# Optimization experiments

Measured on AMD Instinct MI355X. Metric: run time of the kernel, lower is better.

## Reference

```python
import jax, jax.numpy as jnp
import numpy as np

B, S, D, H = 1, 2048, 1024, 16
DH = D // H  # 64
ROPE_THETA = 10000.0


def _rope_tables(seq_len, half_dim, theta):
    inv = 1.0 / (theta ** (np.arange(0, half_dim, dtype=np.float32) / half_dim))
    ang = np.arange(seq_len, dtype=np.float32)[:, None] * inv[None, :]
    return jnp.asarray(np.cos(ang)), jnp.asarray(np.sin(ang))


def setup_inputs() -> dict:
    key = jax.random.key(0)
    ks = jax.random.split(key, 6)
    x = jax.random.normal(ks[0], (B, S, D), dtype=jnp.float32)
    # block-diagonal mask over ~4 packed images -> sorted segment ids
    seg_ids = jnp.sort(jax.random.randint(ks[1], (S,), 0, 4, dtype=jnp.int32))
    freqs_cos, freqs_sin = _rope_tables(S, DH // 2, ROPE_THETA)
    scale = 1.0 / np.sqrt(D)
    wq = jax.random.normal(ks[2], (D, D), dtype=jnp.float32) * scale
    wk = jax.random.normal(ks[3], (D, D), dtype=jnp.float32) * scale
    wv = jax.random.normal(ks[4], (D, D), dtype=jnp.float32) * scale
    wo = jax.random.normal(ks[5], (D, D), dtype=jnp.float32) * scale
    return {"x": x, "seg_ids": seg_ids, "freqs_cos": freqs_cos,
            "freqs_sin": freqs_sin, "wq": wq, "wk": wk, "wv": wv, "wo": wo}


def _apply_rope(t, cos, sin):
    # t: [B,S,H,DH]; interpret last dim as DH//2 complex pairs (real, imag)
    tr = t.reshape(B, S, H, DH // 2, 2)
    a, b = tr[..., 0], tr[..., 1]
    c = cos[None, :, None, :]  # [1,S,1,DH/2]
    s = sin[None, :, None, :]
    out = jnp.stack([a * c - b * s, a * s + b * c], axis=-1)
    return out.reshape(B, S, H, DH)


def reference(x, seg_ids, freqs_cos, freqs_sin, wq, wk, wv, wo):
    q = (x @ wq.T).reshape(B, S, H, DH)
    k = (x @ wk.T).reshape(B, S, H, DH)
    v = (x @ wv.T).reshape(B, S, H, DH)
    q = _apply_rope(q, freqs_cos, freqs_sin)
    k = _apply_rope(k, freqs_cos, freqs_sin)
    scores = jnp.einsum('bqhd,bkhd->bhqk', q, k) / np.float32(np.sqrt(DH))
    block_mask = (seg_ids[:, None] == seg_ids[None, :])  # [S,S] block-diagonal
    scores = jnp.where(block_mask[None, None], scores, jnp.float32(-1e9))
    attn = jax.nn.softmax(scores, axis=-1)
    out = jnp.einsum('bhqk,bkhd->bqhd', attn, v).reshape(B, S, D)
    return out @ wo.T
```

## Files before the change

### kernel.cpp

```cpp
#include <hip/hip_runtime.h>

typedef __bf16 bf16;
typedef __bf16 bf16x4 __attribute__((ext_vector_type(4)));
typedef __bf16 bf16x8 __attribute__((ext_vector_type(8)));
typedef float  f32x4  __attribute__((ext_vector_type(4)));
typedef _Float16 f16;
typedef f16 f16x4 __attribute__((ext_vector_type(4)));

#define S_LEN 2048
#define D_DIM 1024
#define NHEAD 16
#define DHEAD 64
#define NPAR 2

__device__ __forceinline__ void async_cp16(const bf16* g, bf16* l) {
  __builtin_amdgcn_global_load_lds(
      (__attribute__((address_space(1))) void*)(void*)g,
      (__attribute__((address_space(3))) void*)l,
      16, 0, 0);
}

__global__ __launch_bounds__(256) void cvt_k(
    const float* __restrict__ x,  const float* __restrict__ w0,
    const float* __restrict__ w1, const float* __restrict__ w2,
    const float* __restrict__ w3, bf16* __restrict__ dst,
    const int* __restrict__ seg, int* __restrict__ kbr)
{
  __shared__ int firstv[4];
  const int b = blockIdx.x;
  const int t = threadIdx.x;

  if (b < 3072) {
    int i = b * 256 + t;
    const float* src;
    int off;
    if (i < (1 << 18)) {
      src = x; off = i;
    } else {
      int j = i - (1 << 18);
      int s = j >> 17;
      off = j & ((1 << 17) - 1);
      src = (s == 0) ? w0 : (s == 1) ? w1 : (s == 2) ? w2 : w3;
    }
    f32x4 a = *(const f32x4*)(src + (size_t)off * 8);
    f32x4 bb = *(const f32x4*)(src + (size_t)off * 8 + 4);
    bf16x8 o;
    o[0] = (bf16)a[0];  o[1] = (bf16)a[1];  o[2] = (bf16)a[2];  o[3] = (bf16)a[3];
    o[4] = (bf16)bb[0]; o[5] = (bf16)bb[1]; o[6] = (bf16)bb[2]; o[7] = (bf16)bb[3];
    *((bf16x8*)dst + i) = o;
  } else {
    if (t < 4) firstv[t] = S_LEN;
    __syncthreads();
    for (int i = t; i < S_LEN; i += 256) {
      int s = seg[i];
      if (i == 0 || seg[i - 1] != s) atomicMin(&firstv[s], i);
    }
    __syncthreads();
    if (t < 32) {
      int smin = seg[t * 64], smax = seg[t * 64 + 63];
      int lb = S_LEN, ub = S_LEN;
      for (int vv = smin; vv < 4; ++vv) lb = min(lb, firstv[vv]);
      for (int vv = smax + 1; vv < 4; ++vv) ub = min(ub, firstv[vv]);
      kbr[t * 2] = lb >> 6;
      kbr[t * 2 + 1] = (ub - 1) >> 6;
    }
  }
}

__global__ __launch_bounds__(256) void gemm_qkv(
    const bf16* __restrict__ A,
    const bf16* __restrict__ B0, const bf16* __restrict__ B1,
    const bf16* __restrict__ B2,
    const float* __restrict__ cosT, const float* __restrict__ sinT,
    bf16* __restrict__ Cbase, bf16* __restrict__ Vt)
{
  constexpr int K = 1024, N = 1024;
  const int z = blockIdx.z;
  const bf16* W = (z == 0) ? B0 : (z == 1) ? B1 : B2;
  bf16* C = Cbase + (size_t)z * 2048 * 1024;

  __shared__ bf16 As[4][128 * 32] __attribute__((aligned(16)));
  __shared__ bf16 Bs[4][64 * 32] __attribute__((aligned(16)));

  const int t = threadIdx.x;
  const int lane = t & 63;
  const int w = t >> 6;
  const int lm = lane & 15, lq = lane >> 4;
  const int wr = w >> 1, wc = w & 1;
  const int bm = blockIdx.y, bn = blockIdx.x;

  const bf16* Abase = A + (size_t)bm * 128 * K;
  const bf16* Wbase = W + (size_t)bn * 64 * K;

  f32x4 acc[4][2] = {};

  for (int kk = 0; kk < K; kk += 128) {
#pragma unroll
    for (int kh = 0; kh < 2; ++kh)
#pragma unroll
      for (int g = 0; g < 2; ++g) {
        int c = (w * 2 + g) * 64 + lane;
        int row = c >> 2, k8 = c & 3;
        const bf16* ga = Abase + (size_t)row * K + kk + kh * 64 + k8 * 8;
        async_cp16(ga, &As[kh * 2][(w * 2 + g) * 512]);
        async_cp16(ga + 32, &As[kh * 2 + 1][(w * 2 + g) * 512]);
      }
#pragma unroll
    for (int kh = 0; kh < 2; ++kh) {
      int c = w * 64 + lane;
      int row = c >> 2, k8 = c & 3;
      const bf16* gb = Wbase + (size_t)row * K + kk + kh * 64 + k8 * 8;
      async_cp16(gb, &Bs[kh * 2][w * 512]);
      async_cp16(gb + 32, &Bs[kh * 2 + 1][w * 512]);
    }
    __syncthreads();

#pragma unroll
    for (int ks = 0; ks < 4; ++ks) {
      bf16x8 af[4], bfr[2];
#pragma unroll
      for (int mi = 0; mi < 4; ++mi)
        af[mi] = *(const bf16x8*)&As[ks][(wr * 64 + mi * 16 + lm) * 32 + lq * 8];
#pragma unroll
      for (int ni = 0; ni < 2; ++ni)
        bfr[ni] = *(const bf16x8*)&Bs[ks][(wc * 32 + ni * 16 + lm) * 32 + lq * 8];
#pragma unroll
      for (int mi = 0; mi < 4; ++mi)
#pragma unroll
        for (int ni = 0; ni < 2; ++ni)
          acc[mi][ni] = __builtin_amdgcn_mfma_f32_16x16x32_bf16(
              af[mi], bfr[ni], acc[mi][ni], 0, 0, 0);
    }
    __syncthreads();
  }

  if (z < 2) {
    const float scale = (z == 0) ? 0.125f : 1.0f;
#pragma unroll
    for (int mi = 0; mi < 4; ++mi)
#pragma unroll
      for (int ni = 0; ni < 2; ++ni) {
        int gcol = bn * 64 + wc * 32 + ni * 16 + lm;
        int p = (gcol & 63) >> 1;
        bool even = (gcol & 1) == 0;
#pragma unroll
        for (int r = 0; r < 4; ++r) {
          int row = bm * 128 + wr * 64 + mi * 16 + lq * 4 + r;
          float v = acc[mi][ni][r];
          float mate = __shfl_xor(v, 1);
          float cv = cosT[row * 32 + p];
          float sv = sinT[row * 32 + p];
          float res = even ? (v * cv - mate * sv) : (mate * sv + v * cv);
          C[(size_t)row * N + gcol] = (bf16)(res * scale);
        }
      }
  } else {
#pragma unroll
    for (int mi = 0; mi < 4; ++mi)
#pragma unroll
      for (int ni = 0; ni < 2; ++ni) {
        int gcol = bn * 64 + wc * 32 + ni * 16 + lm;
        int rowb = bm * 128 + wr * 64 + mi * 16 + lq * 4;
        bf16x4 pack;
#pragma unroll
        for (int r = 0; r < 4; ++r) pack[r] = (bf16)acc[mi][ni][r];
        *(bf16x4*)(Vt + (size_t)gcol * S_LEN + rowb) = pack;
      }
  }
}

__global__ __launch_bounds__(256) void gemm_wo(
    const bf16* __restrict__ A, const bf16* __restrict__ W,
    float* __restrict__ C)
{
  constexpr int K = 1024, N = 1024;

  __shared__ bf16 As[4][64 * 32] __attribute__((aligned(16)));
  __shared__ bf16 Bs[4][64 * 32] __attribute__((aligned(16)));

  const int t = threadIdx.x;
  const int lane = t & 63;
  const int w = t >> 6;
  const int lm = lane & 15, lq = lane >> 4;
  const int bn = blockIdx.x, bm = blockIdx.y;

  const bf16* Abase = A + (size_t)bm * 64 * K;
  const bf16* Wbase = W + (size_t)bn * 64 * K;

  f32x4 acc[4] = {};

  for (int kk = 0; kk < K; kk += 128) {
#pragma unroll
    for (int kh = 0; kh < 2; ++kh) {
      int c = w * 64 + lane;
      int row = c >> 2, k8 = c & 3;
      const bf16* ga = Abase + (size_t)row * K + kk + kh * 64 + k8 * 8;
      async_cp16(ga, &As[kh * 2][w * 512]);
      async_cp16(ga + 32, &As[kh * 2 + 1][w * 512]);
      const bf16* gb = Wbase + (size_t)row * K + kk + kh * 64 + k8 * 8;
      async_cp16(gb, &Bs[kh * 2][w * 512]);
      async_cp16(gb + 32, &Bs[kh * 2 + 1][w * 512]);
    }
    __syncthreads();

#pragma unroll
    for (int ks = 0; ks < 4; ++ks) {
      bf16x8 af = *(const bf16x8*)&As[ks][(w * 16 + lm) * 32 + lq * 8];
      bf16x8 bfr[4];
#pragma unroll
      for (int ni = 0; ni < 4; ++ni)
        bfr[ni] = *(const bf16x8*)&Bs[ks][(ni * 16 + lm) * 32 + lq * 8];
#pragma unroll
      for (int ni = 0; ni < 4; ++ni)
        acc[ni] = __builtin_amdgcn_mfma_f32_16x16x32_bf16(
            af, bfr[ni], acc[ni], 0, 0, 0);
    }
    __syncthreads();
  }

#pragma unroll
  for (int ni = 0; ni < 4; ++ni) {
    int col = bn * 64 + ni * 16 + lm;
#pragma unroll
    for (int r = 0; r < 4; ++r) {
      int row = bm * 64 + w * 16 + lq * 4 + r;
      C[(size_t)row * N + col] = acc[ni][r];
    }
  }
}

__global__ __launch_bounds__(512, 4) void attn_k(
    const bf16* __restrict__ Q, const bf16* __restrict__ Kmat,
    const bf16* __restrict__ Vt, const int* __restrict__ seg,
    const int* __restrict__ kbr,
    f16* __restrict__ Opar, float* __restrict__ Lpar)
{
  __shared__ bf16 Ks[64 * 72] __attribute__((aligned(16)));
  __shared__ bf16 Vs[64 * 72] __attribute__((aligned(16)));
  __shared__ bf16 Ps[8][16 * 72] __attribute__((aligned(16)));
  __shared__ int segk[64];

  const int h = blockIdx.y;
  const int qt = blockIdx.x & 15, par = blockIdx.x >> 4;
  const int q0 = qt * 128;
  const int t = threadIdx.x, lane = t & 63, w = t >> 6;
  const int lm = lane & 15, lq = lane >> 4;
  const int qrow = q0 + w * 16;

  const int kb0f = kbr[qt * 4], kb1f = kbr[qt * 4 + 3];

  bf16x8 qf[2];
#pragma unroll
  for (int ks = 0; ks < 2; ++ks)
    qf[ks] = *(const bf16x8*)(Q + (size_t)(qrow + lm) * D_DIM + h * DHEAD +
                              ks * 32 + lq * 8);

  int sq[4];
  float l_i[4];
#pragma unroll
  for (int r = 0; r < 4; ++r) {
    sq[r] = seg[qrow + lq * 4 + r];
    l_i[r] = 0.0f;
  }
  f32x4 o[4] = {};

  const int srow0 = t >> 3, sch = (t & 7) * 8;

  const int kbS = kb0f + par;
  f32x4 pk0, pv0;
  int psg;
  if (kbS <= kb1f) {
    const int k0 = kbS * 64;
    pk0 = *(const f32x4*)(Kmat + (size_t)(k0 + srow0) * D_DIM + h * DHEAD + sch);
    pv0 = *(const f32x4*)(Vt + (size_t)(h * DHEAD + srow0) * S_LEN + k0 + sch);
    if (t < 64) psg = seg[k0 + t];
  }

  for (int kb = kbS; kb <= kb1f; kb += NPAR) {
    __syncthreads();
    *(f32x4*)&Ks[srow0 * 72 + sch] = pk0;
    *(f32x4*)&Vs[srow0 * 72 + sch] = pv0;
    if (t < 64) segk[t] = psg;
    __syncthreads();

    if (kb + NPAR <= kb1f) {
      const int k0 = (kb + NPAR) * 64;
      pk0 = *(const f32x4*)(Kmat + (size_t)(k0 + srow0) * D_DIM + h * DHEAD + sch);
      pv0 = *(const f32x4*)(Vt + (size_t)(h * DHEAD + srow0) * S_LEN + k0 + sch);
      if (t < 64) psg = seg[k0 + t];
    }

    f32x4 sa[4] = {};
#pragma unroll
    for (int ks = 0; ks < 2; ++ks) {
      bf16x8 kf[4];
#pragma unroll
      for (int ni = 0; ni < 4; ++ni)
        kf[ni] = *(const bf16x8*)&Ks[(ni * 16 + lm) * 72 + ks * 32 + lq * 8];
#pragma unroll
      for (int ni = 0; ni < 4; ++ni)
        sa[ni] = __builtin_amdgcn_mfma_f32_16x16x32_bf16(qf[ks], kf[ni],
                                                         sa[ni], 0, 0, 0);
    }

    int sk[4];
#pragma unroll
    for (int ni = 0; ni < 4; ++ni) sk[ni] = segk[ni * 16 + lm];

#pragma unroll
    for (int r = 0; r < 4; ++r)
#pragma unroll
      for (int ni = 0; ni < 4; ++ni) {
        float p = (sq[r] == sk[ni]) ? __expf(sa[ni][r]) : 0.0f;
        l_i[r] += p;
        Ps[w][(lq * 4 + r) * 72 + ni * 16 + lm] = (bf16)p;
      }

#pragma unroll
    for (int ks = 0; ks < 2; ++ks) {
      bf16x8 pf = *(const bf16x8*)&Ps[w][lm * 72 + ks * 32 + lq * 8];
      bf16x8 vf[4];
#pragma unroll
      for (int ni = 0; ni < 4; ++ni)
        vf[ni] = *(const bf16x8*)&Vs[(ni * 16 + lm) * 72 + ks * 32 + lq * 8];
#pragma unroll
      for (int ni = 0; ni < 4; ++ni)
        o[ni] = __builtin_amdgcn_mfma_f32_16x16x32_bf16(pf, vf[ni], o[ni],
                                                        0, 0, 0);
    }
  }

  f16* Ob = Opar + ((size_t)(par * NHEAD + h) * S_LEN) * DHEAD;
  float* Lb = Lpar + (size_t)(par * NHEAD + h) * S_LEN;
#pragma unroll
  for (int r = 0; r < 4; ++r) {
    float l = l_i[r];
    l += __shfl_xor(l, 1);
    l += __shfl_xor(l, 2);
    l += __shfl_xor(l, 4);
    l += __shfl_xor(l, 8);
    int row = qrow + lq * 4 + r;
    if (lm == 0) Lb[row] = l;
#pragma unroll
    for (int ni = 0; ni < 4; ++ni)
      Ob[(size_t)row * DHEAD + ni * 16 + lm] = (f16)o[ni][r];
  }
}

__global__ __launch_bounds__(256) void combine_k(
    const f16* __restrict__ Opar, const float* __restrict__ Lpar,
    bf16* __restrict__ AO)
{
  int idx = blockIdx.x * 256 + threadIdx.x;
  int c4 = idx & 15;
  int rh = idx >> 4;
  int row = rh & 2047;
  int h = rh >> 11;
  const size_t PO = (size_t)NHEAD * S_LEN * DHEAD;
  const size_t PL = (size_t)NHEAD * S_LEN;
  const f16* o0 = Opar + ((size_t)h * S_LEN + row) * DHEAD + c4 * 4;
  f32x4 s = {0.f, 0.f, 0.f, 0.f};
  float l = 0.f;
#pragma unroll
  for (int p = 0; p < NPAR; ++p) {
    f16x4 v = *(const f16x4*)(o0 + p * PO);
#pragma unroll
    for (int j = 0; j < 4; ++j) s[j] += (float)v[j];
    l += Lpar[p * PL + (size_t)h * S_LEN + row];
  }
  float inv = 1.0f / l;
  bf16x4 ov;
#pragma unroll
  for (int j = 0; j < 4; ++j) ov[j] = (bf16)(s[j] * inv);
  *(bf16x4*)(AO + (size_t)row * D_DIM + h * DHEAD + c4 * 4) = ov;
}

extern "C" void kernel_launch(void* const* d_in, const int* in_sizes, int n_in,
                              void* d_out, int out_size, void* d_ws,
                              size_t ws_size, hipStream_t stream)
{
  const float* x  = (const float*)d_in[0];
  const int*   sg = (const int*)d_in[1];
  const float* fc = (const float*)d_in[2];
  const float* fs = (const float*)d_in[3];
  const float* wq = (const float*)d_in[4];
  const float* wk = (const float*)d_in[5];
  const float* wv = (const float*)d_in[6];
  const float* wo = (const float*)d_in[7];
  float* out = (float*)d_out;

  const size_t MAT = (size_t)S_LEN * D_DIM;
  const size_t WSZ = (size_t)D_DIM * D_DIM;
  bf16* xb  = (bf16*)d_ws;
  bf16* wqb = xb + MAT;
  bf16* wkb = wqb + WSZ;
  bf16* wvb = wkb + WSZ;
  bf16* wob = wvb + WSZ;
  bf16* q0  = wob + WSZ;
  bf16* k0  = q0 + MAT;
  bf16* vt  = k0 + MAT;
  bf16* ao  = vt + MAT;
  f16*  opar = (f16*)(ao + MAT);
  float* lpar = (float*)(opar + (size_t)NPAR * MAT);
  int*   kbr  = (int*)(lpar + (size_t)NPAR * NHEAD * S_LEN);

  dim3 blk(256);
  cvt_k<<<dim3(3073), blk, 0, stream>>>(x, wq, wk, wv, wo, xb, sg, kbr);
  gemm_qkv<<<dim3(16, 16, 3), blk, 0, stream>>>(xb, wqb, wkb, wvb, fc, fs,
                                                q0, vt);
  attn_k<<<dim3(16 * NPAR, 16), dim3(512), 0, stream>>>(q0, k0, vt, sg, kbr,
                                                        opar, lpar);
  combine_k<<<dim3(2048), blk, 0, stream>>>(opar, lpar, ao);
  gemm_wo<<<dim3(16, 32), blk, 0, stream>>>(ao, wob, out);
}
```

Baseline: 140.8 us.

## Fuse split-KV combine into output projection GEMM and raise MFMA wave priority

Removes the separate combine kernel. The output-projection GEMM now reads both fp16 partial attention outputs and the softmax denominators directly, normalises them and packs bf16 A tiles into shared memory. This saves a launch and a round trip of the intermediate bf16 attention output. The cost is that each of the 16 column blocks recomputes the same combine for its row tile, and the A-tile loads become synchronous register loads instead of async LDS copies. It also adds s_setprio around the MFMA sections in the attention kernel to favour matrix-issuing waves.

```diff
diff --git a/kernel.cpp b/kernel.cpp
--- a/kernel.cpp
+++ b/kernel.cpp
@@ -170,13 +170,16 @@
 }
 
 __global__ __launch_bounds__(256) void gemm_wo(
-    const bf16* __restrict__ A, const bf16* __restrict__ W,
-    float* __restrict__ C)
+    const f16* __restrict__ Opar, const float* __restrict__ Lpar,
+    const bf16* __restrict__ W, float* __restrict__ C)
 {
   constexpr int K = 1024, N = 1024;
+  const size_t PO = (size_t)NHEAD * S_LEN * DHEAD;
+  const size_t PL = (size_t)NHEAD * S_LEN;
 
   __shared__ bf16 As[4][64 * 32] __attribute__((aligned(16)));
   __shared__ bf16 Bs[4][64 * 32] __attribute__((aligned(16)));
+  __shared__ float Linv[NHEAD][64];
 
   const int t = threadIdx.x;
   const int lane = t & 63;
@@ -184,8 +187,14 @@
   const int lm = lane & 15, lq = lane >> 4;
   const int bn = blockIdx.x, bm = blockIdx.y;
 
-  const bf16* Abase = A + (size_t)bm * 64 * K;
   const bf16* Wbase = W + (size_t)bn * 64 * K;
+
+  for (int i = t; i < NHEAD * 64; i += 256) {
+    int h = i >> 6, row = i & 63;
+    size_t li = (size_t)h * S_LEN + bm * 64 + row;
+    Linv[h][row] = 1.0f / (Lpar[li] + Lpar[PL + li]);
+  }
+  __syncthreads();
 
   f32x4 acc[4] = {};
 
@@ -194,12 +203,29 @@
     for (int kh = 0; kh < 2; ++kh) {
       int c = w * 64 + lane;
       int row = c >> 2, k8 = c & 3;
-      const bf16* ga = Abase + (size_t)row * K + kk + kh * 64 + k8 * 8;
-      async_cp16(ga, &As[kh * 2][w * 512]);
-      async_cp16(ga + 32, &As[kh * 2 + 1][w * 512]);
       const bf16* gb = Wbase + (size_t)row * K + kk + kh * 64 + k8 * 8;
       async_cp16(gb, &Bs[kh * 2][w * 512]);
       async_cp16(gb + 32, &Bs[kh * 2 + 1][w * 512]);
+    }
+#pragma unroll
+    for (int p = 0; p < 4; ++p) {
+      int id = p * 256 + t;
+      int row = id >> 4, ch = id & 15;
+      int col = kk + ch * 8;
+      int h = col >> 6, d = col & 63;
+      const f16* o0 = Opar + ((size_t)h * S_LEN + bm * 64 + row) * DHEAD + d;
+      f16x4 a0 = *(const f16x4*)o0;
+      f16x4 a1 = *(const f16x4*)(o0 + 4);
+      f16x4 b0 = *(const f16x4*)(o0 + PO);
+      f16x4 b1 = *(const f16x4*)(o0 + PO + 4);
+      float inv = Linv[h][row];
+      bf16x8 pk;
+#pragma unroll
+      for (int j = 0; j < 4; ++j) {
+        pk[j]     = (bf16)(((float)a0[j] + (float)b0[j]) * inv);
+        pk[4 + j] = (bf16)(((float)a1[j] + (float)b1[j]) * inv);
+      }
+      *(bf16x8*)&As[ch >> 2][row * 32 + (ch & 3) * 8] = pk;
     }
     __syncthreads();
 
@@ -291,6 +317,7 @@
     }
 
     f32x4 sa[4] = {};
+    __builtin_amdgcn_s_setprio(1);
 #pragma unroll
     for (int ks = 0; ks < 2; ++ks) {
       bf16x8 kf[4];
@@ -302,6 +329,7 @@
         sa[ni] = __builtin_amdgcn_mfma_f32_16x16x32_bf16(qf[ks], kf[ni],
                                                          sa[ni], 0, 0, 0);
     }
+    __builtin_amdgcn_s_setprio(0);
 
     int sk[4];
 #pragma unroll
@@ -316,6 +344,7 @@
         Ps[w][(lq * 4 + r) * 72 + ni * 16 + lm] = (bf16)p;
       }
 
+    __builtin_amdgcn_s_setprio(1);
 #pragma unroll
     for (int ks = 0; ks < 2; ++ks) {
       bf16x8 pf = *(const bf16x8*)&Ps[w][lm * 72 + ks * 32 + lq * 8];
@@ -328,6 +357,7 @@
         o[ni] = __builtin_amdgcn_mfma_f32_16x16x32_bf16(pf, vf[ni], o[ni],
                                                         0, 0, 0);
     }
+    __builtin_amdgcn_s_setprio(0);
   }
 
   f16* Ob = Opar + ((size_t)(par * NHEAD + h) * S_LEN) * DHEAD;
@@ -345,34 +375,6 @@
     for (int ni = 0; ni < 4; ++ni)
       Ob[(size_t)row * DHEAD + ni * 16 + lm] = (f16)o[ni][r];
   }
-}
-
-__global__ __launch_bounds__(256) void combine_k(
-    const f16* __restrict__ Opar, const float* __restrict__ Lpar,
-    bf16* __restrict__ AO)
-{
-  int idx = blockIdx.x * 256 + threadIdx.x;
-  int c4 = idx & 15;
-  int rh = idx >> 4;
-  int row = rh & 2047;
-  int h = rh >> 11;
-  const size_t PO = (size_t)NHEAD * S_LEN * DHEAD;
-  const size_t PL = (size_t)NHEAD * S_LEN;
-  const f16* o0 = Opar + ((size_t)h * S_LEN + row) * DHEAD + c4 * 4;
-  f32x4 s = {0.f, 0.f, 0.f, 0.f};
-  float l = 0.f;
-#pragma unroll
-  for (int p = 0; p < NPAR; ++p) {
-    f16x4 v = *(const f16x4*)(o0 + p * PO);
-#pragma unroll
-    for (int j = 0; j < 4; ++j) s[j] += (float)v[j];
-    l += Lpar[p * PL + (size_t)h * S_LEN + row];
-  }
-  float inv = 1.0f / l;
-  bf16x4 ov;
-#pragma unroll
-  for (int j = 0; j < 4; ++j) ov[j] = (bf16)(s[j] * inv);
-  *(bf16x4*)(AO + (size_t)row * D_DIM + h * DHEAD + c4 * 4) = ov;
 }
 
 extern "C" void kernel_launch(void* const* d_in, const int* in_sizes, int n_in,
@@ -399,8 +401,7 @@
   bf16* q0  = wob + WSZ;
   bf16* k0  = q0 + MAT;
   bf16* vt  = k0 + MAT;
-  bf16* ao  = vt + MAT;
-  f16*  opar = (f16*)(ao + MAT);
+  f16*  opar = (f16*)(vt + MAT);
   float* lpar = (float*)(opar + (size_t)NPAR * MAT);
   int*   kbr  = (int*)(lpar + (size_t)NPAR * NHEAD * S_LEN);
 
@@ -410,6 +411,5 @@
                                                 q0, vt);
   attn_k<<<dim3(16 * NPAR, 16), dim3(512), 0, stream>>>(q0, k0, vt, sg, kbr,
                                                         opar, lpar);
-  combine_k<<<dim3(2048), blk, 0, stream>>>(opar, lpar, ao);
-  gemm_wo<<<dim3(16, 32), blk, 0, stream>>>(ao, wob, out);
-}
+  gemm_wo<<<dim3(16, 32), blk, 0, stream>>>(opar, lpar, wob, out);
+}
```

Result: slower. 147.5 us (+4.7%).

## Drop split-K attention partials and combine kernel; normalize output in attention

Applied to the files above, without the earlier changes.

Removes the two-way split over key blocks in the attention kernel and the separate combine kernel. Each block now walks all its key blocks, normalizes by the row sum and writes bf16 output directly. This drops the partial-output and row-sum writes, their later reread, and one kernel launch. The grid shrinks from 512 to 256 blocks, which may leave compute units underused on a large GPU. It also adds s_setprio around the MFMA sections and lowers the launch-bounds occupancy hint.

```diff
diff --git a/kernel.cpp b/kernel.cpp
--- a/kernel.cpp
+++ b/kernel.cpp
@@ -4,14 +4,11 @@
 typedef __bf16 bf16x4 __attribute__((ext_vector_type(4)));
 typedef __bf16 bf16x8 __attribute__((ext_vector_type(8)));
 typedef float  f32x4  __attribute__((ext_vector_type(4)));
-typedef _Float16 f16;
-typedef f16 f16x4 __attribute__((ext_vector_type(4)));
 
 #define S_LEN 2048
 #define D_DIM 1024
 #define NHEAD 16
 #define DHEAD 64
-#define NPAR 2
 
 __device__ __forceinline__ void async_cp16(const bf16* g, bf16* l) {
   __builtin_amdgcn_global_load_lds(
@@ -229,11 +226,11 @@
   }
 }
 
-__global__ __launch_bounds__(512, 4) void attn_k(
+__global__ __launch_bounds__(512, 2) void attn_k(
     const bf16* __restrict__ Q, const bf16* __restrict__ Kmat,
     const bf16* __restrict__ Vt, const int* __restrict__ seg,
     const int* __restrict__ kbr,
-    f16* __restrict__ Opar, float* __restrict__ Lpar)
+    bf16* __restrict__ AO)
 {
   __shared__ bf16 Ks[64 * 72] __attribute__((aligned(16)));
   __shared__ bf16 Vs[64 * 72] __attribute__((aligned(16)));
@@ -241,7 +238,7 @@
   __shared__ int segk[64];
 
   const int h = blockIdx.y;
-  const int qt = blockIdx.x & 15, par = blockIdx.x >> 4;
+  const int qt = blockIdx.x;
   const int q0 = qt * 128;
   const int t = threadIdx.x, lane = t & 63, w = t >> 6;
   const int lm = lane & 15, lq = lane >> 4;
@@ -266,31 +263,31 @@
 
   const int srow0 = t >> 3, sch = (t & 7) * 8;
 
-  const int kbS = kb0f + par;
   f32x4 pk0, pv0;
   int psg;
-  if (kbS <= kb1f) {
-    const int k0 = kbS * 64;
+  {
+    const int k0 = kb0f * 64;
     pk0 = *(const f32x4*)(Kmat + (size_t)(k0 + srow0) * D_DIM + h * DHEAD + sch);
     pv0 = *(const f32x4*)(Vt + (size_t)(h * DHEAD + srow0) * S_LEN + k0 + sch);
     if (t < 64) psg = seg[k0 + t];
   }
 
-  for (int kb = kbS; kb <= kb1f; kb += NPAR) {
+  for (int kb = kb0f; kb <= kb1f; ++kb) {
     __syncthreads();
     *(f32x4*)&Ks[srow0 * 72 + sch] = pk0;
     *(f32x4*)&Vs[srow0 * 72 + sch] = pv0;
     if (t < 64) segk[t] = psg;
     __syncthreads();
 
-    if (kb + NPAR <= kb1f) {
-      const int k0 = (kb + NPAR) * 64;
+    if (kb + 1 <= kb1f) {
+      const int k0 = (kb + 1) * 64;
       pk0 = *(const f32x4*)(Kmat + (size_t)(k0 + srow0) * D_DIM + h * DHEAD + sch);
       pv0 = *(const f32x4*)(Vt + (size_t)(h * DHEAD + srow0) * S_LEN + k0 + sch);
       if (t < 64) psg = seg[k0 + t];
     }
 
     f32x4 sa[4] = {};
+    __builtin_amdgcn_s_setprio(1);
 #pragma unroll
     for (int ks = 0; ks < 2; ++ks) {
       bf16x8 kf[4];
@@ -302,6 +299,7 @@
         sa[ni] = __builtin_amdgcn_mfma_f32_16x16x32_bf16(qf[ks], kf[ni],
                                                          sa[ni], 0, 0, 0);
     }
+    __builtin_amdgcn_s_setprio(0);
 
     int sk[4];
 #pragma unroll
@@ -316,6 +314,7 @@
         Ps[w][(lq * 4 + r) * 72 + ni * 16 + lm] = (bf16)p;
       }
 
+    __builtin_amdgcn_s_setprio(1);
 #pragma unroll
     for (int ks = 0; ks < 2; ++ks) {
       bf16x8 pf = *(const bf16x8*)&Ps[w][lm * 72 + ks * 32 + lq * 8];
@@ -328,10 +327,9 @@
         o[ni] = __builtin_amdgcn_mfma_f32_16x16x32_bf16(pf, vf[ni], o[ni],
                                                         0, 0, 0);
     }
-  }
-
-  f16* Ob = Opar + ((size_t)(par * NHEAD + h) * S_LEN) * DHEAD;
-  float* Lb = Lpar + (size_t)(par * NHEAD + h) * S_LEN;
+    __builtin_amdgcn_s_setprio(0);
+  }
+
 #pragma unroll
   for (int r = 0; r < 4; ++r) {
     float l = l_i[r];
@@ -339,40 +337,13 @@
     l += __shfl_xor(l, 2);
     l += __shfl_xor(l, 4);
     l += __shfl_xor(l, 8);
+    float inv = 1.0f / l;
     int row = qrow + lq * 4 + r;
-    if (lm == 0) Lb[row] = l;
 #pragma unroll
     for (int ni = 0; ni < 4; ++ni)
-      Ob[(size_t)row * DHEAD + ni * 16 + lm] = (f16)o[ni][r];
-  }
-}
-
-__global__ __launch_bounds__(256) void combine_k(
-    const f16* __restrict__ Opar, const float* __restrict__ Lpar,
-    bf16* __restrict__ AO)
-{
-  int idx = blockIdx.x * 256 + threadIdx.x;
-  int c4 = idx & 15;
-  int rh = idx >> 4;
-  int row = rh & 2047;
-  int h = rh >> 11;
-  const size_t PO = (size_t)NHEAD * S_LEN * DHEAD;
-  const size_t PL = (size_t)NHEAD * S_LEN;
-  const f16* o0 = Opar + ((size_t)h * S_LEN + row) * DHEAD + c4 * 4;
-  f32x4 s = {0.f, 0.f, 0.f, 0.f};
-  float l = 0.f;
-#pragma unroll
-  for (int p = 0; p < NPAR; ++p) {
-    f16x4 v = *(const f16x4*)(o0 + p * PO);
-#pragma unroll
-    for (int j = 0; j < 4; ++j) s[j] += (float)v[j];
-    l += Lpar[p * PL + (size_t)h * S_LEN + row];
-  }
-  float inv = 1.0f / l;
-  bf16x4 ov;
-#pragma unroll
-  for (int j = 0; j < 4; ++j) ov[j] = (bf16)(s[j] * inv);
-  *(bf16x4*)(AO + (size_t)row * D_DIM + h * DHEAD + c4 * 4) = ov;
+      AO[(size_t)row * D_DIM + h * DHEAD + ni * 16 + lm] =
+          (bf16)(o[ni][r] * inv);
+  }
 }
 
 extern "C" void kernel_launch(void* const* d_in, const int* in_sizes, int n_in,
@@ -400,16 +371,12 @@
   bf16* k0  = q0 + MAT;
   bf16* vt  = k0 + MAT;
   bf16* ao  = vt + MAT;
-  f16*  opar = (f16*)(ao + MAT);
-  float* lpar = (float*)(opar + (size_t)NPAR * MAT);
-  int*   kbr  = (int*)(lpar + (size_t)NPAR * NHEAD * S_LEN);
+  int*  kbr = (int*)(ao + MAT);
 
   dim3 blk(256);
   cvt_k<<<dim3(3073), blk, 0, stream>>>(x, wq, wk, wv, wo, xb, sg, kbr);
   gemm_qkv<<<dim3(16, 16, 3), blk, 0, stream>>>(xb, wqb, wkb, wvb, fc, fs,
                                                 q0, vt);
-  attn_k<<<dim3(16 * NPAR, 16), dim3(512), 0, stream>>>(q0, k0, vt, sg, kbr,
-                                                        opar, lpar);
-  combine_k<<<dim3(2048), blk, 0, stream>>>(opar, lpar, ao);
+  attn_k<<<dim3(16, 16), dim3(512), 0, stream>>>(q0, k0, vt, sg, kbr, ao);
   gemm_wo<<<dim3(16, 32), blk, 0, stream>>>(ao, wob, out);
 }
```

Result: faster. 136.8 us (-2.9%).
